# Kernel optimization log

Hardware: AMD Instinct MI355X
Metric: run time of the kernel (lower is better)

## Reference

```python
import jax, jax.numpy as jnp
import numpy as np
import math

HEADS = 8
DIM_HEAD = 64
NUM_BUCKETS = 32
MAX_DISTANCE = 128


def _relative_position_bucket(relative_position, num_buckets=NUM_BUCKETS, max_distance=MAX_DISTANCE):
    # T5-style bucketing, faithful to RelativePositionBias._relative_position_bucket
    n = -relative_position
    num_buckets = num_buckets // 2
    ret = (n < 0).astype(jnp.int32) * num_buckets
    n = jnp.abs(n)
    max_exact = num_buckets // 2
    is_small = n < max_exact
    # guard log(0); those lanes are masked out by is_small
    val_if_large = max_exact + (
        jnp.log(jnp.maximum(n, 1).astype(jnp.float32) / max_exact)
        / math.log(max_distance / max_exact)
        * (num_buckets - max_exact)
    ).astype(jnp.int32)
    val_if_large = jnp.minimum(val_if_large, num_buckets - 1)
    return ret + jnp.where(is_small, n, val_if_large)


def _time_rel_pos_bias(n_frames, table):
    pos = jnp.arange(n_frames, dtype=jnp.int32)
    rel_pos = pos[None, :] - pos[:, None]           # [f, f] = k_pos - q_pos
    buckets = _relative_position_bucket(rel_pos)    # [f, f] int
    values = table[buckets]                         # [f, f, heads]
    return jnp.transpose(values, (2, 0, 1))         # [heads, f, f]


def setup_inputs() -> dict:
    key = jax.random.key(0)
    ks = jax.random.split(key, 7)
    B, F, C = 8192, 16, 512
    s = 1.0 / math.sqrt(C)
    return {
        "hidden_states": jax.random.normal(ks[0], (B, F, C), jnp.float32),
        "Wq": jax.random.normal(ks[1], (C, C), jnp.float32) * s,
        "Wk": jax.random.normal(ks[2], (C, C), jnp.float32) * s,
        "Wv": jax.random.normal(ks[3], (C, C), jnp.float32) * s,
        "Wo": jax.random.normal(ks[4], (C, C), jnp.float32) * s,
        "bo": jnp.zeros((C,), jnp.float32),
        "rel_bias_table": jax.random.normal(ks[5], (NUM_BUCKETS, HEADS), jnp.float32) * 0.02,
    }


def reference(hidden_states, Wq, Wk, Wv, Wo, bo, rel_bias_table):
    # hidden_states: [B, F, C] where B = batch*spatial, F = n_frames
    b, f, c = hidden_states.shape
    scale = DIM_HEAD ** -0.5

    q = hidden_states @ Wq  # [B, F, C]
    k = hidden_states @ Wk
    v = hidden_states @ Wv

    def split_heads(t):  # [B, F, C] -> [B, H, F, Dh]
        return t.reshape(b, f, HEADS, DIM_HEAD).transpose(0, 2, 1, 3)

    q, k, v = split_heads(q), split_heads(k), split_heads(v)

    bias = _time_rel_pos_bias(f, rel_bias_table)  # [H, F, F]
    scores = jnp.einsum('bhid,bhjd->bhij', q, k) * scale + bias[None]
    probs = jax.nn.softmax(scores, axis=-1)
    out = jnp.einsum('bhij,bhjd->bhid', probs, v)  # [B, H, F, Dh]
    out = out.transpose(0, 2, 1, 3).reshape(b, f, HEADS * DIM_HEAD)
    return out @ Wo + bo
```

## Files before the change

### kernel.cpp

```cpp
#include <hip/hip_runtime.h>
#include <stdint.h>

typedef unsigned short u16;
typedef __attribute__((ext_vector_type(8))) __bf16 bf16x8;
typedef __attribute__((ext_vector_type(4))) float f32x4;

#define GLOBAL_AS __attribute__((address_space(1)))
#define LDS_AS __attribute__((address_space(3)))

__device__ __forceinline__ float bf2f(u16 v) {
  union { uint32_t u; float f; } x; x.u = (uint32_t)v << 16; return x.f;
}
__device__ __forceinline__ u16 f2bf(float f) {
  union { float f; uint32_t u; } x; x.f = f;
  uint32_t u = x.u + 0x7fffu + ((x.u >> 16) & 1u);
  return (u16)(u >> 16);
}

__global__ void pack_weights(const float* __restrict__ Wq, const float* __restrict__ Wk,
                             const float* __restrict__ Wv, const float* __restrict__ Wo,
                             u16* __restrict__ WT) {
  int g = blockIdx.x * 256 + threadIdx.x;
  int n = g >> 9;
  int k = g & 511;
  const float* src = (n < 1024) ? ((n < 512) ? Wq : Wk) : ((n < 1536) ? Wv : Wo);
  WT[g] = f2bf(src[k * 512 + (n & 511)]);
}

__global__ __launch_bounds__(256) void convert_bf16(const float* __restrict__ src,
                                                    u16* __restrict__ dst) {
  long i = ((long)blockIdx.x * 256 + threadIdx.x) * 8;
  float4 a = *(const float4*)(src + i);
  float4 b = *(const float4*)(src + i + 4);
  uint4 w;
  w.x = (uint32_t)f2bf(a.x) | ((uint32_t)f2bf(a.y) << 16);
  w.y = (uint32_t)f2bf(a.z) | ((uint32_t)f2bf(a.w) << 16);
  w.z = (uint32_t)f2bf(b.x) | ((uint32_t)f2bf(b.y) << 16);
  w.w = (uint32_t)f2bf(b.z) | ((uint32_t)f2bf(b.w) << 16);
  *(uint4*)(dst + i) = w;
}

template <bool AF32, bool CF32>
__global__ __launch_bounds__(256, 2) void gemm_core(
    const void* __restrict__ Ap, int lda,
    const u16* __restrict__ BT,
    const float* __restrict__ bias,
    void* __restrict__ Cp, int ldc)
{
  __shared__ __align__(16) u16 lsA[128 * 32];
  __shared__ __align__(16) u16 lsB[128 * 32];

  const int tid  = threadIdx.x;
  const int wave = tid >> 6;
  const int lane = tid & 63;
  const int quad = lane >> 4;
  const int lrow = lane & 15;
  const int wm = wave & 1;
  const int wn = wave >> 1;

  const long m0 = (long)blockIdx.y * 128;
  const int  n0 = blockIdx.x * 128;

  const int s0 = tid, s1 = 256 + tid;
  const u16* bgp0 = BT + (long)(n0 + (s0 >> 2)) * 512 + (s0 & 3) * 8;
  const u16* bgp1 = BT + (long)(n0 + (s1 >> 2)) * 512 + (s1 & 3) * 8;
  u16* lB0 = lsB + wave * 512;
  u16* lB1 = lsB + 2048 + wave * 512;

  const float* agf0 = (const float*)Ap + (m0 + (s0 >> 2)) * (long)lda + (s0 & 3) * 8;
  const float* agf1 = (const float*)Ap + (m0 + (s1 >> 2)) * (long)lda + (s1 & 3) * 8;
  const u16*   agb0 = (const u16*)Ap + (m0 + (s0 >> 2)) * (long)lda + (s0 & 3) * 8;
  const u16*   agb1 = (const u16*)Ap + (m0 + (s1 >> 2)) * (long)lda + (s1 & 3) * 8;
  u16* lA0 = lsA + wave * 512;
  u16* lA1 = lsA + 2048 + wave * 512;

  f32x4 acc[4][4] = {};

  for (int k0 = 0; k0 < 512; k0 += 32) {
    __syncthreads();
    if constexpr (AF32) {
      float4 x0 = *(const float4*)(agf0 + k0);
      float4 x1 = *(const float4*)(agf0 + k0 + 4);
      float4 y0 = *(const float4*)(agf1 + k0);
      float4 y1 = *(const float4*)(agf1 + k0 + 4);
      uint4 w0, w1;
      w0.x = (uint32_t)f2bf(x0.x) | ((uint32_t)f2bf(x0.y) << 16);
      w0.y = (uint32_t)f2bf(x0.z) | ((uint32_t)f2bf(x0.w) << 16);
      w0.z = (uint32_t)f2bf(x1.x) | ((uint32_t)f2bf(x1.y) << 16);
      w0.w = (uint32_t)f2bf(x1.z) | ((uint32_t)f2bf(x1.w) << 16);
      w1.x = (uint32_t)f2bf(y0.x) | ((uint32_t)f2bf(y0.y) << 16);
      w1.y = (uint32_t)f2bf(y0.z) | ((uint32_t)f2bf(y0.w) << 16);
      w1.z = (uint32_t)f2bf(y1.x) | ((uint32_t)f2bf(y1.y) << 16);
      w1.w = (uint32_t)f2bf(y1.z) | ((uint32_t)f2bf(y1.w) << 16);
      *(uint4*)(lsA + s0 * 8) = w0;
      *(uint4*)(lsA + s1 * 8) = w1;
    } else {
      __builtin_amdgcn_global_load_lds((GLOBAL_AS const uint32_t*)(agb0 + k0),
                                       (LDS_AS uint32_t*)lA0, 16, 0, 0);
      __builtin_amdgcn_global_load_lds((GLOBAL_AS const uint32_t*)(agb1 + k0),
                                       (LDS_AS uint32_t*)lA1, 16, 0, 0);
    }
    __builtin_amdgcn_global_load_lds((GLOBAL_AS const uint32_t*)(bgp0 + k0),
                                     (LDS_AS uint32_t*)lB0, 16, 0, 0);
    __builtin_amdgcn_global_load_lds((GLOBAL_AS const uint32_t*)(bgp1 + k0),
                                     (LDS_AS uint32_t*)lB1, 16, 0, 0);
    __syncthreads();

    bf16x8 af[4], bfr[4];
#pragma unroll
    for (int t = 0; t < 4; ++t) {
      af[t]  = *(const bf16x8*)(lsA + (wm * 64 + t * 16 + lrow) * 32 + quad * 8);
      bfr[t] = *(const bf16x8*)(lsB + (wn * 64 + t * 16 + lrow) * 32 + quad * 8);
    }
#pragma unroll
    for (int mt = 0; mt < 4; ++mt)
#pragma unroll
      for (int nt = 0; nt < 4; ++nt)
        acc[mt][nt] = __builtin_amdgcn_mfma_f32_16x16x32_bf16(af[mt], bfr[nt],
                                                              acc[mt][nt], 0, 0, 0);
  }

#pragma unroll
  for (int mt = 0; mt < 4; ++mt) {
    long rbase = m0 + wm * 64 + mt * 16 + quad * 4;
#pragma unroll
    for (int nt = 0; nt < 4; ++nt) {
      int colg = n0 + wn * 64 + nt * 16 + lrow;
      float badd = bias ? bias[colg] : 0.0f;
      f32x4 v = acc[mt][nt];
#pragma unroll
      for (int r = 0; r < 4; ++r) {
        if constexpr (CF32)
          ((float*)Cp)[(rbase + r) * (long)ldc + colg] = v[r] + badd;
        else
          ((u16*)Cp)[(rbase + r) * (long)ldc + colg] = f2bf(v[r] + badd);
      }
    }
  }
}

#define RS 1544

__global__ __launch_bounds__(256) void attn_k(
    u16* __restrict__ qkv, const float* __restrict__ table )
{
  __shared__ __align__(16) u16 sQ[16 * RS];
  __shared__ float S[8 * 16 * 16];
  const int tid = threadIdx.x;
  const long base = (long)blockIdx.x * (16 * 1536);

  {
    const uint4* src = (const uint4*)(qkv + base);
    uint4* dst = (uint4*)sQ;
#pragma unroll
    for (int r = 0; r < 12; ++r) {
      int idx = r * 256 + tid;
      int row = idx / 192;
      int c   = idx - row * 192;
      dst[row * 193 + c] = src[idx];
    }
  }
  __syncthreads();

  {
    const int h = tid >> 5;
    const int slot = tid & 31;
    const int j = slot & 15;
    const int ibase = (slot >> 4) * 8;
    float kr[64];
    const u16* kp = sQ + j * RS + 512 + h * 64;
#pragma unroll
    for (int d = 0; d < 64; d += 2) {
      uint32_t u = *(const uint32_t*)(kp + d);
      kr[d] = bf2f((u16)u); kr[d + 1] = bf2f((u16)(u >> 16));
    }
#pragma unroll
    for (int r = 0; r < 8; ++r) {
      int i = ibase + r;
      const u16* qp = sQ + i * RS + h * 64;
      float acc = 0.f;
#pragma unroll
      for (int d = 0; d < 64; d += 2) {
        uint32_t u = *(const uint32_t*)(qp + d);
        acc = fmaf(bf2f((u16)u), kr[d], acc);
        acc = fmaf(bf2f((u16)(u >> 16)), kr[d + 1], acc);
      }
      int n = i - j;
      int an = n < 0 ? -n : n;
      int bb = an < 8 ? an : (an < 12 ? 8 : 9);
      int bucket = (n < 0 ? 16 : 0) + bb;
      S[(h * 16 + i) * 16 + j] = acc * 0.125f + table[bucket * 8 + h];
    }
  }
  __syncthreads();

  if (tid < 128) {
    float* row = S + tid * 16;
    float m = row[0];
#pragma unroll
    for (int j = 1; j < 16; ++j) m = fmaxf(m, row[j]);
    float e[16]; float s = 0.f;
#pragma unroll
    for (int j = 0; j < 16; ++j) { e[j] = __expf(row[j] - m); s += e[j]; }
    float inv = 1.0f / s;
#pragma unroll
    for (int j = 0; j < 16; ++j) row[j] = e[j] * inv;
  }
  __syncthreads();

#pragma unroll 4
  for (int r = 0; r < 32; ++r) {
    int e = r * 256 + tid;
    int f = e >> 9;
    int c = e & 511;
    int h = c >> 6;
    const float* p = S + (h * 16 + f) * 16;
    float acc = 0.f;
#pragma unroll
    for (int jj = 0; jj < 16; ++jj)
      acc = fmaf(p[jj], bf2f(sQ[jj * RS + 1024 + c]), acc);
    qkv[base + f * 1536 + c] = f2bf(acc);
  }
}

extern "C" void kernel_launch(void* const* d_in, const int* in_sizes, int n_in,
                              void* d_out, int out_size, void* d_ws, size_t ws_size,
                              hipStream_t stream) {
  (void)in_sizes; (void)n_in; (void)out_size; (void)ws_size;
  const float* hs = (const float*)d_in[0];
  const float* Wq = (const float*)d_in[1];
  const float* Wk = (const float*)d_in[2];
  const float* Wv = (const float*)d_in[3];
  const float* Wo = (const float*)d_in[4];
  const float* bo = (const float*)d_in[5];
  const float* tb = (const float*)d_in[6];
  float* out = (float*)d_out;

  u16* WT  = (u16*)d_ws;
  u16* qkv = (u16*)((char*)d_ws + (4ull << 20));
  u16* Abf = (u16*)d_out;

  convert_bf16<<<32768, 256, 0, stream>>>(hs, Abf);
  pack_weights<<<4096, 256, 0, stream>>>(Wq, Wk, Wv, Wo, WT);

  dim3 g1(12, 1024);
  gemm_core<false, false><<<g1, 256, 0, stream>>>(Abf, 512, WT, nullptr, qkv, 1536);

  attn_k<<<8192, 256, 0, stream>>>(qkv, tb);

  dim3 g3(4, 1024);
  gemm_core<false, true><<<g3, 256, 0, stream>>>(qkv, 1536, WT + 1536 * 512, bo, out, 512);
}
```

Before: 1.056 ms.

## Remap GEMM blocks for XCD locality and vectorize attention LDS access

```diff
diff --git a/kernel.cpp b/kernel.cpp
--- a/kernel.cpp
+++ b/kernel.cpp
@@ -58,8 +58,12 @@
   const int wm = wave & 1;
   const int wn = wave >> 1;
 
-  const long m0 = (long)blockIdx.y * 128;
-  const int  n0 = blockIdx.x * 128;
+  const int gx = gridDim.x;
+  int bid = blockIdx.y * gx + blockIdx.x;
+  int nwg = gx * gridDim.y;
+  int lb = (nwg & 7) ? bid : ((bid & 7) * (nwg >> 3) + (bid >> 3));
+  const int  n0 = (lb % gx) * 128;
+  const long m0 = (long)(lb / gx) * 128;
 
   const int s0 = tid, s1 = 256 + tid;
   const u16* bgp0 = BT + (long)(n0 + (s0 >> 2)) * 512 + (s0 & 3) * 8;
@@ -168,22 +172,31 @@
     const int j = slot & 15;
     const int ibase = (slot >> 4) * 8;
     float kr[64];
-    const u16* kp = sQ + j * RS + 512 + h * 64;
-#pragma unroll
-    for (int d = 0; d < 64; d += 2) {
-      uint32_t u = *(const uint32_t*)(kp + d);
-      kr[d] = bf2f((u16)u); kr[d + 1] = bf2f((u16)(u >> 16));
+    const uint4* kp = (const uint4*)(sQ + j * RS + 512 + h * 64);
+#pragma unroll
+    for (int t = 0; t < 8; ++t) {
+      uint4 u = kp[t];
+      kr[t * 8 + 0] = bf2f((u16)u.x); kr[t * 8 + 1] = bf2f((u16)(u.x >> 16));
+      kr[t * 8 + 2] = bf2f((u16)u.y); kr[t * 8 + 3] = bf2f((u16)(u.y >> 16));
+      kr[t * 8 + 4] = bf2f((u16)u.z); kr[t * 8 + 5] = bf2f((u16)(u.z >> 16));
+      kr[t * 8 + 6] = bf2f((u16)u.w); kr[t * 8 + 7] = bf2f((u16)(u.w >> 16));
     }
 #pragma unroll
     for (int r = 0; r < 8; ++r) {
       int i = ibase + r;
-      const u16* qp = sQ + i * RS + h * 64;
+      const uint4* qp = (const uint4*)(sQ + i * RS + h * 64);
       float acc = 0.f;
 #pragma unroll
-      for (int d = 0; d < 64; d += 2) {
-        uint32_t u = *(const uint32_t*)(qp + d);
-        acc = fmaf(bf2f((u16)u), kr[d], acc);
-        acc = fmaf(bf2f((u16)(u >> 16)), kr[d + 1], acc);
+      for (int t = 0; t < 8; ++t) {
+        uint4 u = qp[t];
+        acc = fmaf(bf2f((u16)u.x),         kr[t * 8 + 0], acc);
+        acc = fmaf(bf2f((u16)(u.x >> 16)), kr[t * 8 + 1], acc);
+        acc = fmaf(bf2f((u16)u.y),         kr[t * 8 + 2], acc);
+        acc = fmaf(bf2f((u16)(u.y >> 16)), kr[t * 8 + 3], acc);
+        acc = fmaf(bf2f((u16)u.z),         kr[t * 8 + 4], acc);
+        acc = fmaf(bf2f((u16)(u.z >> 16)), kr[t * 8 + 5], acc);
+        acc = fmaf(bf2f((u16)u.w),         kr[t * 8 + 6], acc);
+        acc = fmaf(bf2f((u16)(u.w >> 16)), kr[t * 8 + 7], acc);
       }
       int n = i - j;
       int an = n < 0 ? -n : n;
@@ -208,18 +221,41 @@
   }
   __syncthreads();
 
-#pragma unroll 4
-  for (int r = 0; r < 32; ++r) {
-    int e = r * 256 + tid;
-    int f = e >> 9;
-    int c = e & 511;
-    int h = c >> 6;
-    const float* p = S + (h * 16 + f) * 16;
-    float acc = 0.f;
+  {
+    const int c8 = tid & 63;
+    const int f4 = tid >> 6;
+    const int h = c8 >> 3;
+    uint4 vv[16];
 #pragma unroll
     for (int jj = 0; jj < 16; ++jj)
-      acc = fmaf(p[jj], bf2f(sQ[jj * RS + 1024 + c]), acc);
-    qkv[base + f * 1536 + c] = f2bf(acc);
+      vv[jj] = *(const uint4*)(sQ + jj * RS + 1024 + c8 * 8);
+#pragma unroll
+    for (int ff = 0; ff < 4; ++ff) {
+      int f = f4 * 4 + ff;
+      const f32x4* p = (const f32x4*)(S + (h * 16 + f) * 16);
+      f32x4 p0 = p[0], p1 = p[1], p2 = p[2], p3 = p[3];
+      float acc[8] = {};
+#pragma unroll
+      for (int jj = 0; jj < 16; ++jj) {
+        float pj = (jj < 4) ? p0[jj & 3] : (jj < 8) ? p1[jj & 3]
+                 : (jj < 12) ? p2[jj & 3] : p3[jj & 3];
+        uint4 u = vv[jj];
+        acc[0] = fmaf(pj, bf2f((u16)u.x),         acc[0]);
+        acc[1] = fmaf(pj, bf2f((u16)(u.x >> 16)), acc[1]);
+        acc[2] = fmaf(pj, bf2f((u16)u.y),         acc[2]);
+        acc[3] = fmaf(pj, bf2f((u16)(u.y >> 16)), acc[3]);
+        acc[4] = fmaf(pj, bf2f((u16)u.z),         acc[4]);
+        acc[5] = fmaf(pj, bf2f((u16)(u.z >> 16)), acc[5]);
+        acc[6] = fmaf(pj, bf2f((u16)u.w),         acc[6]);
+        acc[7] = fmaf(pj, bf2f((u16)(u.w >> 16)), acc[7]);
+      }
+      uint4 w;
+      w.x = (uint32_t)f2bf(acc[0]) | ((uint32_t)f2bf(acc[1]) << 16);
+      w.y = (uint32_t)f2bf(acc[2]) | ((uint32_t)f2bf(acc[3]) << 16);
+      w.z = (uint32_t)f2bf(acc[4]) | ((uint32_t)f2bf(acc[5]) << 16);
+      w.w = (uint32_t)f2bf(acc[6]) | ((uint32_t)f2bf(acc[7]) << 16);
+      *(uint4*)(qkv + base + f * 1536 + c8 * 8) = w;
+    }
   }
 }
 
```

New measurement: 1.007 ms. 4.6% less time.
